# Kernel optimization log

Hardware: AMD Instinct MI355X
Metric: run time of the kernel (lower is better)

Reference implementation:

```python
import jax, jax.numpy as jnp
import numpy as np

C = jnp.complex64
I2 = jnp.eye(2, dtype=C)
P0 = jnp.array([[1, 0], [0, 0]], dtype=C)
P1 = jnp.array([[0, 0], [0, 1]], dtype=C)
X = jnp.array([[0, 1], [1, 0]], dtype=C)
N_QUBITS = 4


def u3(w):  # w: (3,) = (theta, phi, lam); PennyLane U3 convention
    th, ph, lm = w[0], w[1], w[2]
    ct = jnp.cos(th / 2).astype(C)
    st = jnp.sin(th / 2).astype(C)
    ep = jnp.exp(1j * ph).astype(C)
    el = jnp.exp(1j * lm).astype(C)
    return jnp.stack([jnp.stack([ct, -el * st]), jnp.stack([ep * st, ep * el * ct])])


def ry(t):
    ct = jnp.cos(t / 2).astype(C)
    st = jnp.sin(t / 2).astype(C)
    return jnp.stack([jnp.stack([ct, -st]), jnp.stack([st, ct])])


def rz(t):
    return jnp.diag(jnp.stack([jnp.exp(-1j * t / 2), jnp.exp(1j * t / 2)]).astype(C))


def embed(ops):
    # kron over wires 0..3, wire 0 most significant (PennyLane ordering)
    m = jnp.ones((1, 1), dtype=C)
    for w in range(N_QUBITS):
        m = jnp.kron(m, ops.get(w, I2))
    return m


def cnot(c, t):
    return embed({c: P0}) + embed({c: P1, t: X})


def su4_ops(W, wa, wb):
    # W = (W0..W6): U3,U3,CNOT,RY,RZ,CNOT,RY,CNOT,U3,U3
    return [
        embed({wa: u3(W[0])}),
        embed({wb: u3(W[1])}),
        cnot(wa, wb),
        embed({wa: ry(W[2][0])}),
        embed({wb: rz(W[3][0])}),
        cnot(wb, wa),
        embed({wa: ry(W[4][0])}),
        cnot(wa, wb),
        embed({wa: u3(W[5])}),
        embed({wb: u3(W[6])}),
    ]


def circuit_unitary(weights):
    pairs = [(0, 1), (1, 2), (2, 3), (3, 0)]
    U = jnp.eye(16, dtype=C)
    for Wset in (weights[0:7], weights[7:14]):
        for (a, b) in pairs:
            for g in su4_ops(Wset, a, b):
                U = g @ U
    return U


def setup_inputs() -> dict:
    key = jax.random.key(0)
    ks = jax.random.split(key, 16)
    B = 1048576
    inp = {"patches": jax.random.normal(ks[0], (B, 4), dtype=jnp.float32)}
    sizes = [3, 3, 1, 1, 1, 3, 3, 3, 3, 1, 1, 1, 3, 3]
    for i, s in enumerate(sizes):
        inp[f"weights_{i}"] = jax.random.normal(ks[i + 1], (s,), dtype=jnp.float32)
    return inp


def _forward(patches, weights):
    # sigmoid scaling into [0, pi], then RY AngleEmbedding -> product state
    a = jax.nn.sigmoid(patches) * jnp.float32(np.pi)  # (B, 4)
    c = jnp.cos(a / 2)
    s = jnp.sin(a / 2)
    v = jnp.stack([c, s], axis=-1)  # (B, 4, 2) per-wire single-qubit states
    psi0 = jnp.einsum("bi,bj,bk,bl->bijkl", v[:, 0], v[:, 1], v[:, 2], v[:, 3])
    psi0 = psi0.reshape(-1, 16).astype(C)  # (B, 16), wire 0 most significant
    U = circuit_unitary(weights)  # (16, 16) composed unitary
    psi = psi0 @ U.T  # (B, 16)
    probs = psi.real ** 2 + psi.imag ** 2  # (B, 16) real
    idx = jnp.arange(16)
    bits = (idx[:, None] >> (3 - jnp.arange(4)[None, :])) & 1  # (16, 4)
    signs = (1.0 - 2.0 * bits).astype(probs.dtype)
    return probs @ signs  # (B, 4) <Z_i> expectations


def reference(patches, weights_0, weights_1, weights_2, weights_3, weights_4,
              weights_5, weights_6, weights_7, weights_8, weights_9,
              weights_10, weights_11, weights_12, weights_13):
    weights = [weights_0, weights_1, weights_2, weights_3, weights_4,
               weights_5, weights_6, weights_7, weights_8, weights_9,
               weights_10, weights_11, weights_12, weights_13]
    return _forward(patches, weights)
```

## Files before the change

### kernel.cpp

```cpp
#include <hip/hip_runtime.h>
#include <math.h>


struct cpx { float r, i; };

__device__ inline cpx cmul(cpx a, cpx b) { return {a.r*b.r - a.i*b.i, a.r*b.i + a.i*b.r}; }
__device__ inline cpx cadd(cpx a, cpx b) { return {a.r + b.r, a.i + b.i}; }

template<int BIT>
__device__ inline void apply2(cpx& x, int j, cpx g00, cpx g01, cpx g10, cpx g11) {
  cpx p;
  p.r = __shfl_xor(x.r, BIT, 64);
  p.i = __shfl_xor(x.i, BIT, 64);
  const bool hi = (j & BIT) != 0;
  const cpx ca = hi ? g11 : g00;
  const cpx cb = hi ? g10 : g01;
  x = cadd(cmul(ca, x), cmul(cb, p));
}

template<int CB, int TB>
__device__ inline void cnotg(cpx& x, int j) {
  cpx p;
  p.r = __shfl_xor(x.r, TB, 64);
  p.i = __shfl_xor(x.i, TB, 64);
  if (j & CB) x = p;
}

template<int BIT>
__device__ inline void u3g(cpx& x, int j, float th, float ph, float lm) {
  float st, ct; __sincosf(0.5f * th, &st, &ct);
  float sp, cp; __sincosf(ph, &sp, &cp);
  float sl, cl; __sincosf(lm, &sl, &cl);
  const cpx g00 = { ct, 0.f };
  const cpx g01 = { -cl * st, -sl * st };
  const cpx g10 = {  cp * st,  sp * st };
  const cpx g11 = { (cp*cl - sp*sl) * ct, (sp*cl + cp*sl) * ct };
  apply2<BIT>(x, j, g00, g01, g10, g11);
}

template<int BIT>
__device__ inline void ryg(cpx& x, int j, float t) {
  float s, c; __sincosf(0.5f * t, &s, &c);
  const float pr = __shfl_xor(x.r, BIT, 64);
  const float pi = __shfl_xor(x.i, BIT, 64);
  const float ss = (j & BIT) ? s : -s;
  x.r = fmaf(ss, pr, c * x.r);
  x.i = fmaf(ss, pi, c * x.i);
}

template<int BIT>
__device__ inline void rzg(cpx& x, int j, float t) {
  float s, c; __sincosf(0.5f * t, &s, &c);
  const float ss = (j & BIT) ? s : -s;
  const float nr = fmaf(-ss, x.i, c * x.r);
  const float ni = fmaf( ss, x.r, c * x.i);
  x.r = nr; x.i = ni;
}

template<int A, int B>
__device__ inline void su4g(cpx& x, int j, const float* const* W) {
  constexpr int BA = 8 >> A, BB = 8 >> B;
  u3g<BA>(x, j, W[0][0], W[0][1], W[0][2]);
  u3g<BB>(x, j, W[1][0], W[1][1], W[1][2]);
  cnotg<BA, BB>(x, j);
  ryg<BA>(x, j, W[2][0]);
  rzg<BB>(x, j, W[3][0]);
  cnotg<BB, BA>(x, j);
  ryg<BA>(x, j, W[4][0]);
  cnotg<BA, BB>(x, j);
  u3g<BA>(x, j, W[5][0], W[5][1], W[5][2]);
  u3g<BB>(x, j, W[6][0], W[6][1], W[6][2]);
}

#define BLK 512
#define G   8

#define FORALLG(M) M(0) M(1) M(2) M(3) M(4) M(5) M(6) M(7)
#define FORALLG2(M, jl, jh) M(0,jl,jh) M(1,jl,jh) M(2,jl,jh) M(3,jl,jh) \
                            M(4,jl,jh) M(5,jl,jh) M(6,jl,jh) M(7,jl,jh)

#define DECL_G(g) \
  float ps##g##_0, ps##g##_1, ps##g##_2,  ps##g##_3,  ps##g##_4,  ps##g##_5,  ps##g##_6,  ps##g##_7, \
        ps##g##_8, ps##g##_9, ps##g##_10, ps##g##_11, ps##g##_12, ps##g##_13, ps##g##_14, ps##g##_15; \
  float ax##g = 0.f, ay##g = 0.f, az##g = 0.f, aw##g = 0.f; \
  float re##g, im##g;

#define LOAD_G(g) \
  float4 p##g; \
  { const int e = base + g * BLK; \
    p##g = (e < B) ? pat[e] : make_float4(0.f, 0.f, 0.f, 0.f); }

#define INIT_G(g) { \
  const float h0 = HPI * __builtin_amdgcn_rcpf(1.f + __expf(-p##g.x)); \
  const float h1 = HPI * __builtin_amdgcn_rcpf(1.f + __expf(-p##g.y)); \
  const float h2 = HPI * __builtin_amdgcn_rcpf(1.f + __expf(-p##g.z)); \
  const float h3 = HPI * __builtin_amdgcn_rcpf(1.f + __expf(-p##g.w)); \
  float c0,s0,c1,s1,c2,s2,c3,s3; \
  __sincosf(h0, &s0, &c0); __sincosf(h1, &s1, &c1); \
  __sincosf(h2, &s2, &c2); __sincosf(h3, &s3, &c3); \
  const float a0 = c0*c1, a1 = c0*s1, a2 = s0*c1, a3 = s0*s1; \
  const float b0 = c2*c3, b1 = c2*s3, b2 = s2*c3, b3 = s2*s3; \
  ps##g##_0  = a0*b0; ps##g##_1  = a0*b1; ps##g##_2  = a0*b2; ps##g##_3  = a0*b3; \
  ps##g##_4  = a1*b0; ps##g##_5  = a1*b1; ps##g##_6  = a1*b2; ps##g##_7  = a1*b3; \
  ps##g##_8  = a2*b0; ps##g##_9  = a2*b1; ps##g##_10 = a2*b2; ps##g##_11 = a2*b3; \
  ps##g##_12 = a3*b0; ps##g##_13 = a3*b1; ps##g##_14 = a3*b2; ps##g##_15 = a3*b3; }

#define MUL4(g, jl, jh) \
  re##g = qx * ps##g##_##jl;            im##g = qy * ps##g##_##jl; \
  re##g = fmaf(qz, ps##g##_##jh, re##g); im##g = fmaf(qw, ps##g##_##jh, im##g);
#define FMA4(g, jl, jh) \
  re##g = fmaf(qx, ps##g##_##jl, re##g); im##g = fmaf(qy, ps##g##_##jl, im##g); \
  re##g = fmaf(qz, ps##g##_##jh, re##g); im##g = fmaf(qw, ps##g##_##jh, im##g);

#define STEP(j2, jl, jh, MM) { \
  const float4 q = rowp[j2]; \
  const float qx = q.x, qy = q.y, qz = q.z, qw = q.w; \
  FORALLG2(MM, jl, jh) }

#define ACC_G(g) { \
  const float pr = fmaf(re##g, re##g, im##g * im##g); \
  ax##g = fmaf(s8, pr, ax##g); ay##g = fmaf(s4, pr, ay##g); \
  az##g = fmaf(s2, pr, az##g); aw##g = fmaf(s1, pr, aw##g); }

#define STORE_G(g) { \
  const int e = base + g * BLK; \
  if (e < B) out[e] = make_float4(ax##g, ay##g, az##g, aw##g); }

__global__ __launch_bounds__(BLK, 1)
void quanv_fused(const float4* __restrict__ pat,
                 const float* w0,  const float* w1,  const float* w2,
                 const float* w3,  const float* w4,  const float* w5,
                 const float* w6,  const float* w7,  const float* w8,
                 const float* w9,  const float* w10, const float* w11,
                 const float* w12, const float* w13,
                 float4* __restrict__ out, int B) {
  __shared__ float4 Ush4[128];

  const int tid  = threadIdx.x;
  const int base = blockIdx.x * (BLK * G) + tid;
  const float HPI = 1.5707963267948966f;

  FORALLG(LOAD_G)

  if (tid < 256) {
    const int col = tid >> 4;
    const int j   = tid & 15;
    cpx x = { (j == col) ? 1.f : 0.f, 0.f };
    {
      const float* WA[7] = { w0, w1, w2, w3, w4, w5, w6 };
      su4g<0,1>(x, j, WA); su4g<1,2>(x, j, WA);
      su4g<2,3>(x, j, WA); su4g<3,0>(x, j, WA);
    }
    {
      const float* WB[7] = { w7, w8, w9, w10, w11, w12, w13 };
      su4g<0,1>(x, j, WB); su4g<1,2>(x, j, WB);
      su4g<2,3>(x, j, WB); su4g<3,0>(x, j, WB);
    }
    ((float2*)Ush4)[j * 16 + col] = make_float2(x.r, x.i);
  }
  __syncthreads();

  FORALLG(DECL_G)
  FORALLG(INIT_G)

  for (int k = 0; k < 16; ++k) {
    const float4* __restrict__ rowp = &Ush4[k * 8];
    const float s8 = (k & 8) ? -1.f : 1.f;
    const float s4 = (k & 4) ? -1.f : 1.f;
    const float s2 = (k & 2) ? -1.f : 1.f;
    const float s1 = (k & 1) ? -1.f : 1.f;
    STEP(0,  0,  1, MUL4)
    STEP(1,  2,  3, FMA4)
    STEP(2,  4,  5, FMA4)
    STEP(3,  6,  7, FMA4)
    STEP(4,  8,  9, FMA4)
    STEP(5, 10, 11, FMA4)
    STEP(6, 12, 13, FMA4)
    STEP(7, 14, 15, FMA4)
    FORALLG(ACC_G)
  }

  FORALLG(STORE_G)
}

extern "C" void kernel_launch(void* const* d_in, const int* in_sizes, int n_in,
                              void* d_out, int out_size, void* d_ws, size_t ws_size,
                              hipStream_t stream) {
  (void)n_in; (void)out_size; (void)d_ws; (void)ws_size;
  const int B = in_sizes[0] / 4;
  const int blocks = (B + BLK * G - 1) / (BLK * G);
  for (int rep = 0; rep < 2; ++rep) {
    quanv_fused<<<blocks, BLK, 0, stream>>>(
        (const float4*)d_in[0],
        (const float*)d_in[1],  (const float*)d_in[2],  (const float*)d_in[3],
        (const float*)d_in[4],  (const float*)d_in[5],  (const float*)d_in[6],
        (const float*)d_in[7],  (const float*)d_in[8],  (const float*)d_in[9],
        (const float*)d_in[10], (const float*)d_in[11], (const float*)d_in[12],
        (const float*)d_in[13], (const float*)d_in[14],
        (float4*)d_out, B);
  }
}
```

Measured before the change: 143.7 us.

## Drop duplicate kernel launch and build the two unitary layers in parallel

Removes a redundant second launch of the same kernel, which recomputed identical outputs. The two SU4 layer unitaries are now built concurrently by separate thread halves and combined with a small complex matrix product in shared memory. Patch state initialisation is moved before the barrier so it overlaps the unitary construction. This adds extra shared memory and one more barrier per block.

```diff
diff --git a/kernel.cpp b/kernel.cpp
--- a/kernel.cpp
+++ b/kernel.cpp
@@ -134,6 +134,8 @@
                  const float* w9,  const float* w10, const float* w11,
                  const float* w12, const float* w13,
                  float4* __restrict__ out, int B) {
+  __shared__ float2 L1sh[256];
+  __shared__ float2 L2sh[256];
   __shared__ float4 Ush4[128];
 
   const int tid  = threadIdx.x;
@@ -142,26 +144,41 @@
 
   FORALLG(LOAD_G)
 
-  if (tid < 256) {
-    const int col = tid >> 4;
+  {
+    const int col = (tid & 255) >> 4;
     const int j   = tid & 15;
     cpx x = { (j == col) ? 1.f : 0.f, 0.f };
-    {
-      const float* WA[7] = { w0, w1, w2, w3, w4, w5, w6 };
-      su4g<0,1>(x, j, WA); su4g<1,2>(x, j, WA);
-      su4g<2,3>(x, j, WA); su4g<3,0>(x, j, WA);
+    if (tid < 256) {
+      const float* W[7] = { w0, w1, w2, w3, w4, w5, w6 };
+      su4g<0,1>(x, j, W); su4g<1,2>(x, j, W);
+      su4g<2,3>(x, j, W); su4g<3,0>(x, j, W);
+      L1sh[j * 16 + col] = make_float2(x.r, x.i);
+    } else {
+      const float* W[7] = { w7, w8, w9, w10, w11, w12, w13 };
+      su4g<0,1>(x, j, W); su4g<1,2>(x, j, W);
+      su4g<2,3>(x, j, W); su4g<3,0>(x, j, W);
+      L2sh[j * 16 + col] = make_float2(x.r, x.i);
     }
-    {
-      const float* WB[7] = { w7, w8, w9, w10, w11, w12, w13 };
-      su4g<0,1>(x, j, WB); su4g<1,2>(x, j, WB);
-      su4g<2,3>(x, j, WB); su4g<3,0>(x, j, WB);
+  }
+
+  FORALLG(DECL_G)
+  FORALLG(INIT_G)
+
+  __syncthreads();
+
+  if (tid < 256) {
+    const int k = tid >> 4, c = tid & 15;
+    float ar = 0.f, ai = 0.f;
+#pragma unroll
+    for (int m = 0; m < 16; ++m) {
+      const float2 a = L2sh[k * 16 + m];
+      const float2 b = L1sh[m * 16 + c];
+      ar = fmaf(a.x, b.x, fmaf(-a.y, b.y, ar));
+      ai = fmaf(a.x, b.y, fmaf( a.y, b.x, ai));
     }
-    ((float2*)Ush4)[j * 16 + col] = make_float2(x.r, x.i);
+    ((float2*)Ush4)[k * 16 + c] = make_float2(ar, ai);
   }
   __syncthreads();
-
-  FORALLG(DECL_G)
-  FORALLG(INIT_G)
 
   for (int k = 0; k < 16; ++k) {
     const float4* __restrict__ rowp = &Ush4[k * 8];
@@ -189,14 +206,12 @@
   (void)n_in; (void)out_size; (void)d_ws; (void)ws_size;
   const int B = in_sizes[0] / 4;
   const int blocks = (B + BLK * G - 1) / (BLK * G);
-  for (int rep = 0; rep < 2; ++rep) {
-    quanv_fused<<<blocks, BLK, 0, stream>>>(
-        (const float4*)d_in[0],
-        (const float*)d_in[1],  (const float*)d_in[2],  (const float*)d_in[3],
-        (const float*)d_in[4],  (const float*)d_in[5],  (const float*)d_in[6],
-        (const float*)d_in[7],  (const float*)d_in[8],  (const float*)d_in[9],
-        (const float*)d_in[10], (const float*)d_in[11], (const float*)d_in[12],
-        (const float*)d_in[13], (const float*)d_in[14],
-        (float4*)d_out, B);
-  }
-}
+  quanv_fused<<<blocks, BLK, 0, stream>>>(
+      (const float4*)d_in[0],
+      (const float*)d_in[1],  (const float*)d_in[2],  (const float*)d_in[3],
+      (const float*)d_in[4],  (const float*)d_in[5],  (const float*)d_in[6],
+      (const float*)d_in[7],  (const float*)d_in[8],  (const float*)d_in[9],
+      (const float*)d_in[10], (const float*)d_in[11], (const float*)d_in[12],
+      (const float*)d_in[13], (const float*)d_in[14],
+      (float4*)d_out, B);
+}
```

Result: faster. 118.7 us (-17.3%).
